# Kernel optimization log

Measured on AMD Instinct MI355X. Metric: run time of the kernel, lower is better.

Reference implementation:

```python
import jax, jax.numpy as jnp
import numpy as np

DIM = 192; HEADS = 6; WS = (2, 7, 7); SS = (1, 3, 3)
HEAD_DIM = DIM // HEADS; SCALE = HEAD_DIM ** -0.5
NW_TOK = WS[0] * WS[1] * WS[2]  # 98 tokens per window
HIDDEN = 4 * DIM


def _rel_pos_index():
    d, h, w = WS
    coords = np.stack(np.meshgrid(np.arange(d), np.arange(h), np.arange(w), indexing='ij'))
    cf = coords.reshape(3, -1)
    rc = (cf[:, :, None] - cf[:, None, :]).transpose(1, 2, 0).astype(np.int64)
    rc[:, :, 0] += d - 1; rc[:, :, 1] += h - 1; rc[:, :, 2] += w - 1
    rc[:, :, 0] *= (2 * h - 1) * (2 * w - 1)
    rc[:, :, 1] *= (2 * w - 1)
    return jnp.asarray(rc.sum(-1))  # (98, 98)

REL_IDX = _rel_pos_index()


def layer_norm(x, w, b):
    m = x.mean(-1, keepdims=True)
    v = ((x - m) ** 2).mean(-1, keepdims=True)
    return (x - m) / jnp.sqrt(v + 1e-5) * w + b


def window_partition(x, ws):
    B, D, H, W, C = x.shape
    x = x.reshape(B, D // ws[0], ws[0], H // ws[1], ws[1], W // ws[2], ws[2], C)
    x = x.transpose(0, 1, 3, 5, 2, 4, 6, 7)
    return x.reshape(-1, ws[0] * ws[1] * ws[2], C)


def window_reverse(w, ws, B, D, H, W):
    x = w.reshape(B, D // ws[0], H // ws[1], W // ws[2], ws[0], ws[1], ws[2], -1)
    x = x.transpose(0, 1, 4, 2, 5, 3, 6, 7)
    return x.reshape(B, D, H, W, -1)


def mlp(x, fc1_w, fc1_b, fc2_w, fc2_b):
    return jax.nn.gelu(x @ fc1_w + fc1_b, approximate=False) @ fc2_w + fc2_b


def setup_inputs() -> dict:
    key = jax.random.key(0)
    ks = jax.random.split(key, 16)
    B, D, H, W, C = 2, 8, 56, 56, DIM
    nW = (D // WS[0]) * (H // WS[1]) * (W // WS[2])
    return {
        'x': jax.random.normal(ks[0], (B, D, H, W, C), jnp.float32),
        'global_token': jax.random.normal(ks[1], (B * nW, 1, C), jnp.float32),
        'position': jax.random.normal(ks[2], (B * nW, 1, C), jnp.float32),
        'attn_mask': jax.random.normal(ks[3], (nW, NW_TOK, NW_TOK), jnp.float32),
        'norm1_w': jnp.ones((C,), jnp.float32),
        'norm1_b': jnp.zeros((C,), jnp.float32),
        'qkv_w': jax.random.normal(ks[4], (C, 3 * C), jnp.float32) * 0.02,
        'qkv_b': jnp.zeros((3 * C,), jnp.float32),
        'proj_w': jax.random.normal(ks[5], (C, C), jnp.float32) * 0.02,
        'proj_b': jnp.zeros((C,), jnp.float32),
        'rpb_table': jax.random.normal(ks[6], ((2 * WS[0] - 1) * (2 * WS[1] - 1) * (2 * WS[2] - 1), HEADS), jnp.float32) * 0.02,
        'norm2_w': jnp.ones((C,), jnp.float32),
        'norm2_b': jnp.zeros((C,), jnp.float32),
        'fc1_w': jax.random.normal(ks[7], (C, HIDDEN), jnp.float32) * 0.02,
        'fc1_b': jnp.zeros((HIDDEN,), jnp.float32),
        'fc2_w': jax.random.normal(ks[8], (HIDDEN, C), jnp.float32) * 0.02,
        'fc2_b': jnp.zeros((C,), jnp.float32),
    }


def reference(x, global_token, position, attn_mask, norm1_w, norm1_b, qkv_w, qkv_b,
              proj_w, proj_b, rpb_table, norm2_w, norm2_b, fc1_w, fc1_b, fc2_w, fc2_b):
    B, D, H, W, C = x.shape
    shortcut = x
    xn = layer_norm(x, norm1_w, norm1_b)
    # pad to multiple of window size (static no-op here but kept for fidelity)
    pd, ph, pw = (-D) % WS[0], (-H) % WS[1], (-W) % WS[2]
    xn = jnp.pad(xn, ((0, 0), (0, pd), (0, ph), (0, pw), (0, 0)))
    Dp, Hp, Wp = D + pd, H + ph, W + pw
    xn = jnp.roll(xn, (-SS[0], -SS[1], -SS[2]), axis=(1, 2, 3))
    xw = window_partition(xn, WS)                       # (B*nW, 98, C)
    xw = jnp.concatenate([global_token, xw], axis=1)    # (B*nW, 99, C)
    B_, N, _ = xw.shape
    qkv = (xw @ qkv_w + qkv_b).reshape(B_, N, 3, HEADS, HEAD_DIM).transpose(2, 0, 3, 1, 4)
    q, k, v = qkv[0] * SCALE, qkv[1], qkv[2]
    attn = jnp.einsum('bhnd,bhmd->bhnm', q, k)          # (B_, H, 99, 99)
    rpb = rpb_table[REL_IDX.reshape(-1)].reshape(NW_TOK, NW_TOK, HEADS).transpose(2, 0, 1)
    nW = attn_mask.shape[0]
    extra = rpb[None] + jnp.tile(attn_mask, (B_ // nW, 1, 1))[:, None]
    attn = attn.at[:, :, 1:, 1:].add(extra)
    attn = jax.nn.softmax(attn, axis=-1)
    out = jnp.einsum('bhnm,bhmd->bhnd', attn, v).transpose(0, 2, 1, 3).reshape(B_, N, C)
    out = out @ proj_w + proj_b
    xw, gt = out[:, 1:], out[:, :1]
    xr = window_reverse(xw, WS, B, Dp, Hp, Wp)
    xr = jnp.roll(xr, SS, axis=(1, 2, 3))[:, :D, :H, :W, :]
    x = shortcut + xr
    x = x + mlp(layer_norm(x, norm2_w, norm2_b), fc1_w, fc1_b, fc2_w, fc2_b)
    gt = gt + mlp(layer_norm(gt, norm2_w, norm2_b), fc1_w, fc1_b, fc2_w, fc2_b)
    return (x, gt)
```

## Files before the change

kernel.cpp:

```cpp
#include <hip/hip_runtime.h>
#include <math.h>

typedef float f32x4 __attribute__((ext_vector_type(4)));
typedef __bf16 bf16x4 __attribute__((ext_vector_type(4)));
typedef __bf16 bf16x8 __attribute__((ext_vector_type(8)));

union FragU { bf16x8 v; bf16x4 h[2]; };

__device__ __forceinline__ unsigned short f2bf(float x) {
  union { float f; unsigned u; } un; un.f = x;
  unsigned r = un.u + 0x7FFFu + ((un.u >> 16) & 1u);
  return (unsigned short)(r >> 16);
}
__device__ __forceinline__ float bf2f(unsigned short h) {
  union { unsigned u; float f; } un; un.u = ((unsigned)h) << 16;
  return un.f;
}

__device__ __forceinline__ void gl16(const unsigned short* g, unsigned short* l) {
  __builtin_amdgcn_global_load_lds(
      (const __attribute__((address_space(1))) void*)g,
      (__attribute__((address_space(3))) void*)l, 16, 0, 0);
}

#define MROWS 50688
#define XTOK  50176
#define GT_OFF 9633792
#define SCALE_Q 0.17677669529663687f

__global__ __launch_bounds__(256) void prep_all(
    const float* __restrict__ qkvw, const float* __restrict__ projw,
    const float* __restrict__ fc1w, const float* __restrict__ fc2w,
    const float* __restrict__ amask, const float* __restrict__ rpb,
    unsigned short* __restrict__ wout,
    unsigned int* __restrict__ maskP, unsigned int* __restrict__ rpbP)
{
  __shared__ float M[98][99];
  const int tid = threadIdx.x;
  const int blk = blockIdx.x;
  if (blk < 1728) {
    int idx = blk * 256 + tid;
    float v;
    if (idx < 110592)      { int n = idx / 192, k = idx - n * 192; v = qkvw[k * 576 + n]; }
    else if (idx < 147456) { int j = idx - 110592; int n = j / 192, k = j - n * 192; v = projw[k * 192 + n]; }
    else if (idx < 294912) { int j = idx - 147456; int n = j / 192, k = j - n * 192; v = fc1w[k * 768 + n]; }
    else                   { int j = idx - 294912; int n = j / 768, k = j - n * 768; v = fc2w[k * 192 + n]; }
    wout[idx] = f2bf(v);
  } else if (blk < 1984) {
    const int w256 = blk - 1728;
    const float* src = amask + (size_t)w256 * 9604;
    for (int i = tid; i < 9604; i += 256) {
      int ti = i / 98, tj = i - ti * 98;
      M[ti][tj] = src[i];
    }
    __syncthreads();
    unsigned int* dst = maskP + (size_t)w256 * 6336;
    for (int o = tid; o < 6336; o += 256) {
      int base = o / 396, rem = o - base * 396;
      int t = rem / 99, r = rem - t * 99;
      int c0 = base + 32 * t;
      unsigned int res = 0;
      #pragma unroll
      for (int h = 0; h < 2; h++) {
        int c = c0 + 16 * h;
        float v = 0.0f;
        if (r >= 1 && c >= 1 && c <= 98) v = M[r - 1][c - 1];
        res |= ((unsigned int)f2bf(v)) << (16 * h);
      }
      dst[o] = res;
    }
  } else {
    int idx = (blk - 1984) * 256 + tid;
    if (idx >= 38016) return;
    int head = idx / 6336, o = idx - head * 6336;
    int base = o / 396, rem = o - base * 396;
    int t = rem / 99, r = rem - t * 99;
    int c0 = base + 32 * t;
    unsigned int res = 0;
    #pragma unroll
    for (int h = 0; h < 2; h++) {
      int c = c0 + 16 * h;
      float v = 0.0f;
      if (r >= 1 && c >= 1 && c <= 98) {
        int ti = r - 1, tj = c - 1;
        int tdi = ti / 49, ri = ti - tdi * 49, thi = ri / 7, twi = ri - thi * 7;
        int tdj = tj / 49, rj = tj - tdj * 49, thj = rj / 7, twj = rj - thj * 7;
        int rel = (tdi - tdj + 1) * 169 + (thi - thj + 6) * 13 + (twi - twj + 6);
        v = rpb[rel * 6 + head];
      }
      res |= ((unsigned int)f2bf(v)) << (16 * h);
    }
    rpbP[idx] = res;
  }
}

__global__ __launch_bounds__(256) void ln1_kernel(
    const float* __restrict__ x, const float* __restrict__ gtok,
    const float* __restrict__ lw, const float* __restrict__ lb,
    unsigned short* __restrict__ out)
{
  int row = blockIdx.x * 4 + (threadIdx.x >> 6);
  int lane = threadIdx.x & 63;
  int win = row / 99, t = row - win * 99;
  size_t obase = (size_t)row * 192;
  if (t == 0) {
    const float* src = gtok + (size_t)win * 192;
    out[obase + lane]       = f2bf(src[lane]);
    out[obase + lane + 64]  = f2bf(src[lane + 64]);
    out[obase + lane + 128] = f2bf(src[lane + 128]);
    return;
  }
  int b = win >> 8, wi = win & 255;
  int wd = wi >> 6, wh = (wi >> 3) & 7, ww = wi & 7;
  int tt = t - 1, td = tt / 49, rr = tt - td * 49, th = rr / 7, tw = rr - th * 7;
  int d = (wd * 2 + td + 1) & 7;
  int h = wh * 7 + th + 3; if (h >= 56) h -= 56;
  int wc = ww * 7 + tw + 3; if (wc >= 56) wc -= 56;
  const float* src = x + ((size_t)(((b * 8 + d) * 56 + h) * 56 + wc)) * 192;
  float v0 = src[lane], v1 = src[lane + 64], v2 = src[lane + 128];
  float s = v0 + v1 + v2;
  float ss = v0 * v0 + v1 * v1 + v2 * v2;
  #pragma unroll
  for (int off = 32; off; off >>= 1) { s += __shfl_xor(s, off); ss += __shfl_xor(ss, off); }
  float mean = s * (1.0f / 192.0f);
  float var = ss * (1.0f / 192.0f) - mean * mean;
  float rstd = rsqrtf(var + 1e-5f);
  out[obase + lane]       = f2bf((v0 - mean) * rstd * lw[lane]       + lb[lane]);
  out[obase + lane + 64]  = f2bf((v1 - mean) * rstd * lw[lane + 64]  + lb[lane + 64]);
  out[obase + lane + 128] = f2bf((v2 - mean) * rstd * lw[lane + 128] + lb[lane + 128]);
}

__global__ __launch_bounds__(256) void ln2_kernel(
    const float* __restrict__ resbuf,
    const float* __restrict__ lw, const float* __restrict__ lb,
    unsigned short* __restrict__ out)
{
  int row = blockIdx.x * 4 + (threadIdx.x >> 6);
  int lane = threadIdx.x & 63;
  const float* src = resbuf + (size_t)row * 192;
  float v0 = src[lane], v1 = src[lane + 64], v2 = src[lane + 128];
  float s = v0 + v1 + v2;
  float ss = v0 * v0 + v1 * v1 + v2 * v2;
  #pragma unroll
  for (int off = 32; off; off >>= 1) { s += __shfl_xor(s, off); ss += __shfl_xor(ss, off); }
  float mean = s * (1.0f / 192.0f);
  float var = ss * (1.0f / 192.0f) - mean * mean;
  float rstd = rsqrtf(var + 1e-5f);
  size_t obase = (size_t)row * 192;
  out[obase + lane]       = f2bf((v0 - mean) * rstd * lw[lane]       + lb[lane]);
  out[obase + lane + 64]  = f2bf((v1 - mean) * rstd * lw[lane + 64]  + lb[lane + 64]);
  out[obase + lane + 128] = f2bf((v2 - mean) * rstd * lw[lane + 128] + lb[lane + 128]);
}

template<int MODE>
__global__ __launch_bounds__(256) void gemm_tpl(
    const unsigned short* __restrict__ A,
    const unsigned short* __restrict__ BT,
    const float* __restrict__ bias,
    unsigned short* __restrict__ outb,
    const float* __restrict__ xin,
    float* __restrict__ resbuf,
    float* __restrict__ dout,
    int N, int K, int NC, int NWG)
{
  __shared__ unsigned short As0[128 * 64], As1[128 * 64];
  __shared__ unsigned short Bs0[64 * 64],  Bs1[64 * 64];
  const int tid = threadIdx.x, lane = tid & 63, w = tid >> 6;
  const int wm = w >> 1, wn = w & 1;
  const int l15 = lane & 15, l4 = lane >> 4;
  const int sx = lane & 7;
  const int srow8 = lane >> 3;
  const int csrc = (lane & 7) ^ srow8;

  const int L = blockIdx.x;
  const int xcd = L & 7, hi = L >> 3;
  const int q = NWG >> 3, rr = NWG & 7;
  const int wgid = (xcd < rr ? xcd * (q + 1) : rr * (q + 1) + (xcd - rr) * q) + hi;
  const int cb = wgid % NC, rb = wgid / NC;
  const int mbase = rb * 128, nbase = cb * 64;

  const unsigned short* aSrc[4];
  #pragma unroll
  for (int i = 0; i < 4; i++)
    aSrc[i] = A + (size_t)(mbase + (w * 4 + i) * 8 + srow8) * K + csrc * 8;
  const unsigned short* bSrc[2];
  #pragma unroll
  for (int i = 0; i < 2; i++)
    bSrc[i] = BT + (size_t)(nbase + (w * 2 + i) * 8 + srow8) * K + csrc * 8;

  f32x4 acc[4][2] = {};

  const int kiters = K >> 6;
  #pragma unroll
  for (int i = 0; i < 4; i++) gl16(aSrc[i], As0 + (w * 4 + i) * 512);
  #pragma unroll
  for (int i = 0; i < 2; i++) gl16(bSrc[i], Bs0 + (w * 2 + i) * 512);
  __syncthreads();

  for (int t = 0; t < kiters; t++) {
    unsigned short* aCur = (t & 1) ? As1 : As0;
    unsigned short* bCur = (t & 1) ? Bs1 : Bs0;
    if (t + 1 < kiters) {
      unsigned short* aNxt = (t & 1) ? As0 : As1;
      unsigned short* bNxt = (t & 1) ? Bs0 : Bs1;
      const int kb = (t + 1) * 64;
      #pragma unroll
      for (int i = 0; i < 4; i++) gl16(aSrc[i] + kb, aNxt + (w * 4 + i) * 512);
      #pragma unroll
      for (int i = 0; i < 2; i++) gl16(bSrc[i] + kb, bNxt + (w * 2 + i) * 512);
    }

    #pragma unroll
    for (int ks = 0; ks < 2; ks++) {
      bf16x8 af[4], bfr[2];
      #pragma unroll
      for (int mi = 0; mi < 4; mi++) {
        int r = wm * 64 + mi * 16 + l15;
        af[mi] = *reinterpret_cast<const bf16x8*>(aCur + r * 64 + (((ks * 4 + l4) ^ sx) * 8));
      }
      #pragma unroll
      for (int nj = 0; nj < 2; nj++) {
        int c = wn * 32 + nj * 16 + l15;
        bfr[nj] = *reinterpret_cast<const bf16x8*>(bCur + c * 64 + (((ks * 4 + l4) ^ sx) * 8));
      }
      #pragma unroll
      for (int mi = 0; mi < 4; mi++)
        #pragma unroll
        for (int nj = 0; nj < 2; nj++)
          acc[mi][nj] = __builtin_amdgcn_mfma_f32_16x16x32_bf16(af[mi], bfr[nj], acc[mi][nj], 0, 0, 0);
    }
    if (t + 1 < kiters) __syncthreads();
  }

  #pragma unroll
  for (int mi = 0; mi < 4; mi++)
    #pragma unroll
    for (int nj = 0; nj < 2; nj++)
      #pragma unroll
      for (int reg = 0; reg < 4; reg++) {
        int r = mbase + wm * 64 + mi * 16 + l4 * 4 + reg;
        int c = nbase + wn * 32 + nj * 16 + l15;
        float v = acc[mi][nj][reg] + bias[c];
        if constexpr (MODE == 0) {
          if (c < 192) v *= SCALE_Q;
          outb[(size_t)r * N + c] = f2bf(v);
        } else if constexpr (MODE == 1) {
          int win = r / 99, t2 = r - win * 99;
          if (t2 == 0) {
            resbuf[(size_t)(XTOK + win) * 192 + c] = v;
          } else {
            int b = win >> 8, wi = win & 255;
            int wd = wi >> 6, wh = (wi >> 3) & 7, ww = wi & 7;
            int tt = t2 - 1, td = tt / 49, rr2 = tt - td * 49, th = rr2 / 7, tw = rr2 - th * 7;
            int d = (wd * 2 + td + 1) & 7;
            int h = wh * 7 + th + 3; if (h >= 56) h -= 56;
            int wc = ww * 7 + tw + 3; if (wc >= 56) wc -= 56;
            size_t idx = ((size_t)(((b * 8 + d) * 56 + h) * 56 + wc)) * 192 + c;
            resbuf[idx] = xin[idx] + v;
          }
        } else if constexpr (MODE == 2) {
          float p = v * (1.5957691216f + 0.0713548128f * v * v);
          float g = v * __builtin_amdgcn_rcpf(1.0f + __expf(-p));
          outb[(size_t)r * N + c] = f2bf(g);
        } else {
          v += resbuf[(size_t)r * 192 + c];
          if (r < XTOK) dout[(size_t)r * 192 + c] = v;
          else dout[GT_OFF + (size_t)(r - XTOK) * 192 + c] = v;
        }
      }
}

__global__ __launch_bounds__(256, 4) void attn_kernel(
    const unsigned short* __restrict__ qkv,
    const unsigned int* __restrict__ maskP,
    const unsigned int* __restrict__ rpbP,
    unsigned short* __restrict__ out)
{
  const int win = blockIdx.x & 511;
  const int head = blockIdx.x >> 9;
  const int tid = threadIdx.x, lane = tid & 63, w = tid >> 6;
  const int l15 = lane & 15, l4 = (lane >> 4) & 3;

  __shared__ __align__(16) unsigned short Qs[128][40];
  __shared__ __align__(16) unsigned short Ks[128][40];
  __shared__ __align__(16) unsigned short VTs[32][136];

  const size_t rowbase = (size_t)win * 99;

  const unsigned int* mkb = maskP + (size_t)(win & 255) * 6336;
  const unsigned int* rpb_ = rpbP + (size_t)head * 6336;
  const int q0 = w * 16 + l15;
  const int q1 = 64 + q0;
  const int r1 = q1 < 99 ? q1 : 0;
  unsigned int mk0[4][4], mk1[4][4], rp0[4][4], rp1[4][4];
  #pragma unroll
  for (int reg = 0; reg < 4; reg++)
    #pragma unroll
    for (int t = 0; t < 4; t++) {
      int boff = ((l4 * 4 + reg) * 4 + t) * 99;
      mk0[reg][t] = mkb[boff + q0];
      mk1[reg][t] = mkb[boff + r1];
      rp0[reg][t] = rpb_[boff + q0];
      rp1[reg][t] = rpb_[boff + r1];
    }

  for (int idx = tid; idx < 512; idx += 256) {
    int r = idx >> 2, seg = (idx & 3) * 8;
    int4 zq = {0,0,0,0}, zk = {0,0,0,0}, zv = {0,0,0,0};
    if (r < 99) {
      const unsigned short* src = qkv + (rowbase + r) * 576 + head * 32 + seg;
      zq = *reinterpret_cast<const int4*>(src);
      zk = *reinterpret_cast<const int4*>(src + 192);
      zv = *reinterpret_cast<const int4*>(src + 384);
    }
    *reinterpret_cast<int4*>(&Qs[r][seg]) = zq;
    *reinterpret_cast<int4*>(&Ks[r][seg]) = zk;
    const unsigned short* pv = reinterpret_cast<const unsigned short*>(&zv);
    #pragma unroll
    for (int j = 0; j < 8; j++) VTs[seg + j][r] = pv[j];
  }
  __syncthreads();

  f32x4 oacc[2][2] = {};

  #pragma unroll
  for (int qi = 0; qi < 2; qi++) {
    const int qrow = qi * 64 + w * 16 + l15;
    FragU qf;
    qf.h[0] = *reinterpret_cast<const bf16x4*>(&Qs[qrow][l4 * 4]);
    qf.h[1] = *reinterpret_cast<const bf16x4*>(&Qs[qrow][16 + l4 * 4]);

    f32x4 sacc[7] = {};
    #pragma unroll
    for (int nj = 0; nj < 7; nj++) {
      FragU kf;
      kf.h[0] = *reinterpret_cast<const bf16x4*>(&Ks[nj * 16 + l15][l4 * 4]);
      kf.h[1] = *reinterpret_cast<const bf16x4*>(&Ks[nj * 16 + l15][16 + l4 * 4]);
      sacc[nj] = __builtin_amdgcn_mfma_f32_16x16x32_bf16(kf.v, qf.v, sacc[nj], 0, 0, 0);
    }

    float m = -1e30f;
    #pragma unroll
    for (int nj = 0; nj < 7; nj++) {
      int t = nj >> 1;
      #pragma unroll
      for (int reg = 0; reg < 4; reg++) {
        unsigned int mu = qi ? mk1[reg][t] : mk0[reg][t];
        unsigned int ru = qi ? rp1[reg][t] : rp0[reg][t];
        unsigned int mb = (nj & 1) ? (mu & 0xFFFF0000u) : (mu << 16);
        unsigned int rb = (nj & 1) ? (ru & 0xFFFF0000u) : (ru << 16);
        float s = sacc[nj][reg] + __uint_as_float(mb) + __uint_as_float(rb);
        if (nj == 6 && (96 + l4 * 4 + reg) >= 99) s = -1e30f;
        sacc[nj][reg] = s;
        m = fmaxf(m, s);
      }
    }
    m = fmaxf(m, __shfl_xor(m, 16));
    m = fmaxf(m, __shfl_xor(m, 32));
    float sum = 0.0f;
    #pragma unroll
    for (int nj = 0; nj < 7; nj++)
      #pragma unroll
      for (int reg = 0; reg < 4; reg++) {
        float e = __expf(sacc[nj][reg] - m);
        sacc[nj][reg] = e;
        sum += e;
      }
    sum += __shfl_xor(sum, 16);
    sum += __shfl_xor(sum, 32);
    const float inv = 1.0f / sum;

    #pragma unroll
    for (int ks = 0; ks < 4; ks++) {
      union { unsigned short u[8]; bf16x8 v; } pa;
      #pragma unroll
      for (int j = 0; j < 4; j++) {
        pa.u[j] = f2bf(sacc[2 * ks][j] * inv);
        pa.u[4 + j] = (ks == 3) ? (unsigned short)0 : f2bf(sacc[2 * ks + 1][j] * inv);
      }
      #pragma unroll
      for (int njd = 0; njd < 2; njd++) {
        FragU vb;
        vb.h[0] = *reinterpret_cast<const bf16x4*>(&VTs[njd * 16 + l15][ks * 32 + l4 * 4]);
        vb.h[1] = *reinterpret_cast<const bf16x4*>(&VTs[njd * 16 + l15][ks * 32 + 16 + l4 * 4]);
        oacc[qi][njd] = __builtin_amdgcn_mfma_f32_16x16x32_bf16(pa.v, vb.v, oacc[qi][njd], 0, 0, 0);
      }
    }
  }

  #pragma unroll
  for (int qi = 0; qi < 2; qi++)
    #pragma unroll
    for (int njd = 0; njd < 2; njd++)
      #pragma unroll
      for (int reg = 0; reg < 4; reg++) {
        int q = qi * 64 + w * 16 + l4 * 4 + reg;
        if (q < 99)
          out[(rowbase + q) * 192 + head * 32 + njd * 16 + l15] = f2bf(oacc[qi][njd][reg]);
      }
}

extern "C" void kernel_launch(void* const* d_in, const int* in_sizes, int n_in,
                              void* d_out, int out_size, void* d_ws, size_t ws_size,
                              hipStream_t stream) {
  (void)in_sizes; (void)n_in; (void)out_size; (void)ws_size;
  const float* x     = (const float*)d_in[0];
  const float* gtok  = (const float*)d_in[1];
  const float* amask = (const float*)d_in[3];
  const float* n1w   = (const float*)d_in[4];
  const float* n1b   = (const float*)d_in[5];
  const float* qkvw  = (const float*)d_in[6];
  const float* qkvb  = (const float*)d_in[7];
  const float* projw = (const float*)d_in[8];
  const float* projb = (const float*)d_in[9];
  const float* rpb   = (const float*)d_in[10];
  const float* n2w   = (const float*)d_in[11];
  const float* n2b   = (const float*)d_in[12];
  const float* fc1w  = (const float*)d_in[13];
  const float* fc1b  = (const float*)d_in[14];
  const float* fc2w  = (const float*)d_in[15];
  const float* fc2b  = (const float*)d_in[16];

  char* ws = (char*)d_ws;
  unsigned short* wbuf = (unsigned short*)ws;
  unsigned short* X    = (unsigned short*)(ws + 884736);
  unsigned short* Qb   = (unsigned short*)(ws + 20348928);
  float*          Rb   = (float*)(ws + 98205696);
  unsigned int*   maskP= (unsigned int*)(ws + 98205696);
  unsigned int*   rpbP = (unsigned int*)(ws + 104693760);
  float* dout = (float*)d_out;

  prep_all<<<2133, 256, 0, stream>>>(qkvw, projw, fc1w, fc2w, amask, rpb, wbuf, maskP, rpbP);
  ln1_kernel<<<12672, 256, 0, stream>>>(x, gtok, n1w, n1b, X);
  gemm_tpl<0><<<3564, 256, 0, stream>>>(X, wbuf, qkvb, Qb, nullptr, nullptr, nullptr, 576, 192, 9, 3564);
  attn_kernel<<<3072, 256, 0, stream>>>(Qb, maskP, rpbP, X);
  gemm_tpl<1><<<1188, 256, 0, stream>>>(X, wbuf + 110592, projb, nullptr, x, Rb, nullptr, 192, 192, 3, 1188);
  ln2_kernel<<<12672, 256, 0, stream>>>(Rb, n2w, n2b, X);
  gemm_tpl<2><<<4752, 256, 0, stream>>>(X, wbuf + 147456, fc1b, Qb, nullptr, nullptr, nullptr, 768, 192, 12, 4752);
  gemm_tpl<3><<<1188, 256, 0, stream>>>(Qb, wbuf + 294912, fc2b, nullptr, nullptr, Rb, dout, 192, 768, 3, 1188);
}
```

Before: 197.9 us.

## Widen GEMM N-tile to 96 and drop LDS double buffering

The GEMM tile grows from 128x64 to 128x96, so each wave computes a 4x3 grid of MFMA fragments and every kernel launches fewer workgroups. The A tile is reused across more output columns, which cuts global and LDS traffic per output. The double-buffered LDS prefetch is replaced by single-buffered load, sync, compute. This lowers LDS use and may raise occupancy, but global load latency is no longer overlapped with MFMA work.

```diff
diff --git a/kernel.cpp b/kernel.cpp
--- a/kernel.cpp
+++ b/kernel.cpp
@@ -163,8 +163,8 @@
     float* __restrict__ dout,
     int N, int K, int NC, int NWG)
 {
-  __shared__ unsigned short As0[128 * 64], As1[128 * 64];
-  __shared__ unsigned short Bs0[64 * 64],  Bs1[64 * 64];
+  __shared__ unsigned short As[128 * 64];
+  __shared__ unsigned short Bs[96 * 64];
   const int tid = threadIdx.x, lane = tid & 63, w = tid >> 6;
   const int wm = w >> 1, wn = w & 1;
   const int l15 = lane & 15, l4 = lane >> 4;
@@ -177,56 +177,42 @@
   const int q = NWG >> 3, rr = NWG & 7;
   const int wgid = (xcd < rr ? xcd * (q + 1) : rr * (q + 1) + (xcd - rr) * q) + hi;
   const int cb = wgid % NC, rb = wgid / NC;
-  const int mbase = rb * 128, nbase = cb * 64;
-
-  const unsigned short* aSrc[4];
-  #pragma unroll
-  for (int i = 0; i < 4; i++)
-    aSrc[i] = A + (size_t)(mbase + (w * 4 + i) * 8 + srow8) * K + csrc * 8;
-  const unsigned short* bSrc[2];
-  #pragma unroll
-  for (int i = 0; i < 2; i++)
-    bSrc[i] = BT + (size_t)(nbase + (w * 2 + i) * 8 + srow8) * K + csrc * 8;
-
-  f32x4 acc[4][2] = {};
+  const int mbase = rb * 128, nbase = cb * 96;
+
+  f32x4 acc[4][3] = {};
 
   const int kiters = K >> 6;
-  #pragma unroll
-  for (int i = 0; i < 4; i++) gl16(aSrc[i], As0 + (w * 4 + i) * 512);
-  #pragma unroll
-  for (int i = 0; i < 2; i++) gl16(bSrc[i], Bs0 + (w * 2 + i) * 512);
-  __syncthreads();
-
   for (int t = 0; t < kiters; t++) {
-    unsigned short* aCur = (t & 1) ? As1 : As0;
-    unsigned short* bCur = (t & 1) ? Bs1 : Bs0;
-    if (t + 1 < kiters) {
-      unsigned short* aNxt = (t & 1) ? As0 : As1;
-      unsigned short* bNxt = (t & 1) ? Bs0 : Bs1;
-      const int kb = (t + 1) * 64;
-      #pragma unroll
-      for (int i = 0; i < 4; i++) gl16(aSrc[i] + kb, aNxt + (w * 4 + i) * 512);
-      #pragma unroll
-      for (int i = 0; i < 2; i++) gl16(bSrc[i] + kb, bNxt + (w * 2 + i) * 512);
-    }
+    const int kb = t * 64;
+    #pragma unroll
+    for (int i = 0; i < 4; i++) {
+      int chunk = w * 4 + i;
+      gl16(A + (size_t)(mbase + chunk * 8 + srow8) * K + kb + csrc * 8, As + chunk * 512);
+    }
+    #pragma unroll
+    for (int i = 0; i < 3; i++) {
+      int chunk = w * 3 + i;
+      gl16(BT + (size_t)(nbase + chunk * 8 + srow8) * K + kb + csrc * 8, Bs + chunk * 512);
+    }
+    __syncthreads();
 
     #pragma unroll
     for (int ks = 0; ks < 2; ks++) {
-      bf16x8 af[4], bfr[2];
+      bf16x8 af[4], bfr[3];
       #pragma unroll
       for (int mi = 0; mi < 4; mi++) {
         int r = wm * 64 + mi * 16 + l15;
-        af[mi] = *reinterpret_cast<const bf16x8*>(aCur + r * 64 + (((ks * 4 + l4) ^ sx) * 8));
-      }
-      #pragma unroll
-      for (int nj = 0; nj < 2; nj++) {
-        int c = wn * 32 + nj * 16 + l15;
-        bfr[nj] = *reinterpret_cast<const bf16x8*>(bCur + c * 64 + (((ks * 4 + l4) ^ sx) * 8));
+        af[mi] = *reinterpret_cast<const bf16x8*>(As + r * 64 + (((ks * 4 + l4) ^ sx) * 8));
+      }
+      #pragma unroll
+      for (int nj = 0; nj < 3; nj++) {
+        int c = wn * 48 + nj * 16 + l15;
+        bfr[nj] = *reinterpret_cast<const bf16x8*>(Bs + c * 64 + (((ks * 4 + l4) ^ sx) * 8));
       }
       #pragma unroll
       for (int mi = 0; mi < 4; mi++)
         #pragma unroll
-        for (int nj = 0; nj < 2; nj++)
+        for (int nj = 0; nj < 3; nj++)
           acc[mi][nj] = __builtin_amdgcn_mfma_f32_16x16x32_bf16(af[mi], bfr[nj], acc[mi][nj], 0, 0, 0);
     }
     if (t + 1 < kiters) __syncthreads();
@@ -235,11 +221,11 @@
   #pragma unroll
   for (int mi = 0; mi < 4; mi++)
     #pragma unroll
-    for (int nj = 0; nj < 2; nj++)
+    for (int nj = 0; nj < 3; nj++)
       #pragma unroll
       for (int reg = 0; reg < 4; reg++) {
         int r = mbase + wm * 64 + mi * 16 + l4 * 4 + reg;
-        int c = nbase + wn * 32 + nj * 16 + l15;
+        int c = nbase + wn * 48 + nj * 16 + l15;
         float v = acc[mi][nj][reg] + bias[c];
         if constexpr (MODE == 0) {
           if (c < 192) v *= SCALE_Q;
@@ -432,10 +418,10 @@
 
   prep_all<<<2133, 256, 0, stream>>>(qkvw, projw, fc1w, fc2w, amask, rpb, wbuf, maskP, rpbP);
   ln1_kernel<<<12672, 256, 0, stream>>>(x, gtok, n1w, n1b, X);
-  gemm_tpl<0><<<3564, 256, 0, stream>>>(X, wbuf, qkvb, Qb, nullptr, nullptr, nullptr, 576, 192, 9, 3564);
+  gemm_tpl<0><<<2376, 256, 0, stream>>>(X, wbuf, qkvb, Qb, nullptr, nullptr, nullptr, 576, 192, 6, 2376);
   attn_kernel<<<3072, 256, 0, stream>>>(Qb, maskP, rpbP, X);
-  gemm_tpl<1><<<1188, 256, 0, stream>>>(X, wbuf + 110592, projb, nullptr, x, Rb, nullptr, 192, 192, 3, 1188);
+  gemm_tpl<1><<<792, 256, 0, stream>>>(X, wbuf + 110592, projb, nullptr, x, Rb, nullptr, 192, 192, 2, 792);
   ln2_kernel<<<12672, 256, 0, stream>>>(Rb, n2w, n2b, X);
-  gemm_tpl<2><<<4752, 256, 0, stream>>>(X, wbuf + 147456, fc1b, Qb, nullptr, nullptr, nullptr, 768, 192, 12, 4752);
-  gemm_tpl<3><<<1188, 256, 0, stream>>>(Qb, wbuf + 294912, fc2b, nullptr, nullptr, Rb, dout, 192, 768, 3, 1188);
-}
+  gemm_tpl<2><<<3168, 256, 0, stream>>>(X, wbuf + 147456, fc1b, Qb, nullptr, nullptr, nullptr, 768, 192, 8, 3168);
+  gemm_tpl<3><<<792, 256, 0, stream>>>(Qb, wbuf + 294912, fc2b, nullptr, nullptr, Rb, dout, 192, 768, 2, 792);
+}
```

After: 227.4 us. 14.9% more time.
